# Kernel optimization log

Hardware: AMD Instinct MI355X
Metric: run time of the kernel (lower is better)

The kernel has to match this reference:

```python
import jax, jax.numpy as jnp
from jax import lax
import numpy as np

B, L, D = 2, 2048, 768
DI, DS, DTR, K = 1536, 16, 48, 4  # d_inner, d_state, dt_rank, d_conv
EPS = 1e-5


def layernorm(x, g, b):
    mu = jnp.mean(x, axis=-1, keepdims=True)
    var = jnp.mean(jnp.square(x - mu), axis=-1, keepdims=True)
    return (x - mu) * lax.rsqrt(var + EPS) * g + b


def mamba(x, in_w, conv_w, conv_b, xproj_w, dt_w, dt_b, A_log, Dp, out_w):
    # x: [B, L, D]
    xz = x @ in_w.T                       # [B, L, 2*DI]
    xc, z = jnp.split(xz, 2, axis=-1)     # [B, L, DI] each
    # causal depthwise conv1d, kernel K, left pad K-1, truncate to L
    xp = jnp.pad(xc, ((0, 0), (K - 1, 0), (0, 0)))
    conv = conv_b + sum(xp[:, k:k + L, :] * conv_w[:, k] for k in range(K))
    xc = jax.nn.silu(conv)
    dbc = xc @ xproj_w.T                  # [B, L, DTR+2*DS]
    dt = dbc[..., :DTR]
    Bm = dbc[..., DTR:DTR + DS]           # [B, L, DS]
    Cm = dbc[..., DTR + DS:]              # [B, L, DS]
    dt = jax.nn.softplus(dt @ dt_w.T + dt_b)  # [B, L, DI]
    A = -jnp.exp(A_log)                   # [DI, DS]

    def step(h, inp):
        dt_t, B_t, C_t, x_t = inp         # [B,DI], [B,DS], [B,DS], [B,DI]
        dA = jnp.exp(dt_t[..., None] * A)               # [B, DI, DS]
        h = dA * h + (dt_t * x_t)[..., None] * B_t[:, None, :]
        y = jnp.einsum('bds,bs->bd', h, C_t)
        return h, y

    h0 = jnp.zeros((x.shape[0], DI, DS), x.dtype)
    _, ys = lax.scan(step, h0, (dt.transpose(1, 0, 2), Bm.transpose(1, 0, 2),
                                Cm.transpose(1, 0, 2), xc.transpose(1, 0, 2)))
    y = ys.transpose(1, 0, 2) + xc * Dp   # [B, L, DI]
    y = y * jax.nn.silu(z)
    return y @ out_w.T                    # [B, L, D]


def setup_inputs() -> dict:
    key = jax.random.key(0)
    ks = iter(jax.random.split(key, 40))
    r = lambda s, sc=0.02: jax.random.normal(next(ks), s, jnp.float32) * sc
    A0 = jnp.log(jnp.broadcast_to(jnp.arange(1, DS + 1, dtype=jnp.float32), (DI, DS)))
    def mamba_params(p):
        return {
            f'{p}_in_w': r((2 * DI, D)), f'{p}_conv_w': r((DI, K), 0.2),
            f'{p}_conv_b': jnp.zeros((DI,)), f'{p}_xproj_w': r((DTR + 2 * DS, DI)),
            f'{p}_dt_w': r((DI, DTR), 0.1), f'{p}_dt_b': jnp.zeros((DI,)),
            f'{p}_A_log': A0, f'{p}_D': jnp.ones((DI,)), f'{p}_out_w': r((D, DI)),
        }
    inp = {'x': jax.random.normal(next(ks), (B, L, D), jnp.float32),
           'norm_g': jnp.ones((D,)), 'norm_b': jnp.zeros((D,))}
    inp.update(mamba_params('f'))
    inp.update(mamba_params('b'))
    inp.update({'mix_w': r((D, 2 * D)), 'mix_b': jnp.zeros((D,)),
                'ffn_w1': r((4 * D, D)), 'ffn_b1': jnp.zeros((4 * D,)),
                'ffn_w2': r((D, 4 * D)), 'ffn_b2': jnp.zeros((D,)),
                'ffn_norm_g': jnp.ones((D,)), 'ffn_norm_b': jnp.zeros((D,))})
    return inp


def reference(x, norm_g, norm_b,
              f_in_w, f_conv_w, f_conv_b, f_xproj_w, f_dt_w, f_dt_b, f_A_log, f_D, f_out_w,
              b_in_w, b_conv_w, b_conv_b, b_xproj_w, b_dt_w, b_dt_b, b_A_log, b_D, b_out_w,
              mix_w, mix_b, ffn_w1, ffn_b1, ffn_w2, ffn_b2, ffn_norm_g, ffn_norm_b):
    residual = x
    xn = layernorm(x, norm_g, norm_b)
    xf = mamba(xn, f_in_w, f_conv_w, f_conv_b, f_xproj_w, f_dt_w, f_dt_b, f_A_log, f_D, f_out_w)
    xb = mamba(jnp.flip(xn, axis=1), b_in_w, b_conv_w, b_conv_b, b_xproj_w,
               b_dt_w, b_dt_b, b_A_log, b_D, b_out_w)
    xb = jnp.flip(xb, axis=1)
    xm = jnp.concatenate([xf, xb], axis=-1) @ mix_w.T + mix_b
    h = xm + residual
    hn = layernorm(h, ffn_norm_g, ffn_norm_b)
    ff = jax.nn.gelu(hn @ ffn_w1.T + ffn_b1) @ ffn_w2.T + ffn_b2  # dropout = eval identity
    return ff + h
```

## Files before the change

kernel.cpp:

```cpp
#include <hip/hip_runtime.h>
#include <hip/hip_bf16.h>
#include <math.h>

#define NB 2
#define LL 2048
#define DD 768
#define DI 1536
#define DS 16
#define MM (NB*LL)
#define TCH 64
#define NCH 32
#define CONV_R 8

typedef __hip_bfloat16 bf16;
typedef __attribute__((ext_vector_type(8))) __bf16 bf16x8;
typedef __attribute__((ext_vector_type(4))) float f32x4;

__device__ __forceinline__ float b2f(bf16 v){ return __bfloat162float(v); }
__device__ __forceinline__ bf16 f2b(float v){ return __float2bfloat16(v); }
__device__ __forceinline__ float bu2f(unsigned short u){
  union {unsigned i; float f;} a; a.i = ((unsigned)u) << 16; return a.f;
}

__device__ __forceinline__ void un2(unsigned u, float& lo, float& hi){
  union {unsigned i; float f;} a, b;
  a.i = u << 16; b.i = u & 0xffff0000u;
  lo = a.f; hi = b.f;
}

__device__ __forceinline__ void async_cp16(const bf16* g, __bf16* l) {
  __builtin_amdgcn_global_load_lds((const __attribute__((address_space(1))) void*)g,
                                   (__attribute__((address_space(3))) void*)l, 16, 0, 0);
}

#define ACT_NONE 0
#define ACT_SOFTPLUS 1
#define ACT_GELU 2

__device__ __forceinline__ float apply_act(float v, int act) {
  if (act == ACT_SOFTPLUS) {
    v = (v > 15.f) ? v : log1pf(__expf(v));
  } else if (act == ACT_GELU) {
    float u = 0.7978845608028654f * (v + 0.044715f*v*v*v);
    v = 0.5f * v * (1.f + tanhf(u));
  }
  return v;
}

__global__ __launch_bounds__(512)
void gemm_kernel(const bf16* __restrict__ A, int lda,
                 const bf16* __restrict__ B, int ldb,
                 void* __restrict__ C, int ldc,
                 int N, int K,
                 const float* __restrict__ bias,
                 const float* __restrict__ addp, int ldadd,
                 int act, int f32out)
{
  __shared__ __bf16 As[128*64];
  __shared__ __bf16 Bs[128*64];
  const int tid  = threadIdx.x;
  const int lane = tid & 63, wave = tid >> 6;
  const int m0 = blockIdx.x * 128, n0 = blockIdx.y * 128;
  const int wm = wave >> 2, wn = wave & 3;

  const int srow = tid >> 3;
  const int gsw  = (tid & 7) ^ (srow & 7);
  const int scol = gsw * 8;
  const bf16* Ag[2]; const bf16* Bg[2]; int dstv[2];
  #pragma unroll
  for (int i = 0; i < 2; i++) {
    int r = srow + i*64;
    Ag[i] = A + (size_t)(m0 + r) * lda + scol;
    int br = n0 + r; if (br > N-1) br = N-1;
    Bg[i] = B + (size_t)br * ldb + scol;
    dstv[i] = r*64 + (tid & 7)*8;
  }

  f32x4 acc[4][2] = {};
  const int f = lane & 15, gq = lane >> 4, rx = lane & 7;
  const int abase = wm*64;
  const int bbase = wn*32;

  for (int kb = 0; kb < K; kb += 64) {
    __syncthreads();
    #pragma unroll
    for (int i = 0; i < 2; i++) {
      async_cp16(Ag[i] + kb, &As[dstv[i]]);
      async_cp16(Bg[i] + kb, &Bs[dstv[i]]);
    }
    __syncthreads();
    #pragma unroll
    for (int h = 0; h < 2; h++) {
      const int kk = ((h*4 + gq) ^ rx) * 8;
      bf16x8 af[4], bfr[2];
      #pragma unroll
      for (int i = 0; i < 4; i++) af[i]  = *(const bf16x8*)&As[(abase + i*16 + f)*64 + kk];
      #pragma unroll
      for (int j = 0; j < 2; j++) bfr[j] = *(const bf16x8*)&Bs[(bbase + j*16 + f)*64 + kk];
      #pragma unroll
      for (int i = 0; i < 4; i++)
        #pragma unroll
        for (int j = 0; j < 2; j++)
          acc[i][j] = __builtin_amdgcn_mfma_f32_16x16x32_bf16(af[i], bfr[j], acc[i][j], 0, 0, 0);
    }
  }

  bf16*  Cb = (bf16*)C;
  float* Cf = (float*)C;
  #pragma unroll
  for (int i = 0; i < 4; i++) {
    int rbase = m0 + wm*64 + i*16 + gq*4;
    #pragma unroll
    for (int j = 0; j < 2; j++) {
      int col = n0 + wn*32 + j*16 + f;
      if (col >= N) continue;
      float bv = bias ? bias[col] : 0.f;
      #pragma unroll
      for (int r = 0; r < 4; r++) {
        int row = rbase + r;
        float v = apply_act(acc[i][j][r] + bv, act);
        if (addp) v += addp[(size_t)row * ldadd + col];
        if (f32out) Cf[(size_t)row * ldc + col] = v;
        else        Cb[(size_t)row * ldc + col] = f2b(v);
      }
    }
  }
}

__global__ void gemm64_kernel(const bf16* __restrict__ A, int lda, size_t sA,
                              const bf16* __restrict__ B, int ldb, size_t sB,
                              void* __restrict__ C, int ldc, size_t sC,
                              int N, int K,
                              const float* __restrict__ bias0,
                              const float* __restrict__ bias1, int biasBase,
                              const float* __restrict__ addp, int ldadd,
                              int act, int f32out)
{
  __shared__ __bf16 As[64*64];
  __shared__ __bf16 Bs[64*64];
  const int tid  = threadIdx.x;
  const int lane = tid & 63, wave = tid >> 6;
  const int z = blockIdx.z;
  A += (size_t)z * sA;
  B += (size_t)z * sB;
  const float* bias = ((biasBase + z) ? bias1 : bias0);
  const int m0 = blockIdx.x * 64, n0 = blockIdx.y * 64;
  const int wm = wave & 1, wn = wave >> 1;

  const int srow = wave*16 + (lane >> 3);
  const int gsw  = (lane & 7) ^ ((lane >> 3) & 7);
  const int scol = gsw * 8;
  const bf16* Ag[2]; const bf16* Bg[2];
  __bf16 *AsW[2], *BsW[2];
  #pragma unroll
  for (int i = 0; i < 2; i++) {
    int ar = m0 + srow + i*8;
    Ag[i] = A + (size_t)ar * lda + scol;
    int br = n0 + srow + i*8; if (br > N-1) br = N-1;
    Bg[i] = B + (size_t)br * ldb + scol;
    AsW[i] = &As[(wave*16 + i*8)*64];
    BsW[i] = &Bs[(wave*16 + i*8)*64];
  }

  f32x4 acc[2][2] = {};
  const int arow = wm*32 + (lane & 15);
  const int brow = wn*32 + (lane & 15);
  const int rx = lane & 7;
  const int gq = lane >> 4;

  for (int kb = 0; kb < K; kb += 64) {
    __syncthreads();
    #pragma unroll
    for (int i = 0; i < 2; i++) {
      async_cp16(Ag[i] + kb, AsW[i]);
      async_cp16(Bg[i] + kb, BsW[i]);
    }
    __syncthreads();
    #pragma unroll
    for (int h = 0; h < 2; h++) {
      const int kk = ((h*4 + gq) ^ rx) * 8;
      bf16x8 af[2], bfr[2];
      #pragma unroll
      for (int i = 0; i < 2; i++) af[i]  = *(const bf16x8*)&As[(arow + i*16)*64 + kk];
      #pragma unroll
      for (int j = 0; j < 2; j++) bfr[j] = *(const bf16x8*)&Bs[(brow + j*16)*64 + kk];
      #pragma unroll
      for (int i = 0; i < 2; i++)
        #pragma unroll
        for (int j = 0; j < 2; j++)
          acc[i][j] = __builtin_amdgcn_mfma_f32_16x16x32_bf16(af[i], bfr[j], acc[i][j], 0, 0, 0);
    }
  }

  bf16*  Cb = (bf16*)C + z*sC;
  float* Cf = (float*)C + z*sC;
  #pragma unroll
  for (int i = 0; i < 2; i++) {
    int rbase = m0 + wm*32 + i*16 + (lane >> 4)*4;
    #pragma unroll
    for (int j = 0; j < 2; j++) {
      int col = n0 + wn*32 + j*16 + (lane & 15);
      if (col >= N) continue;
      float bv = bias ? bias[col] : 0.f;
      #pragma unroll
      for (int r = 0; r < 4; r++) {
        int row = rbase + r;
        float v = apply_act(acc[i][j][r] + bv, act);
        if (addp) v += addp[(size_t)row * ldadd + col];
        if (f32out) Cf[(size_t)row * ldc + col] = v;
        else        Cb[(size_t)row * ldc + col] = f2b(v);
      }
    }
  }
}

__global__ void ln_kernel(const float* __restrict__ x, const float* __restrict__ g,
                          const float* __restrict__ b, bf16* __restrict__ out)
{
  const int row = blockIdx.x;
  const int tid = threadIdx.x;
  const float* xr = x + (size_t)row * DD;
  float v[3], s = 0.f, s2 = 0.f;
  #pragma unroll
  for (int i = 0; i < 3; i++) {
    float f = xr[tid + i*256];
    v[i] = f; s += f; s2 += f*f;
  }
  #pragma unroll
  for (int o = 32; o > 0; o >>= 1) { s += __shfl_down(s, o, 64); s2 += __shfl_down(s2, o, 64); }
  __shared__ float ps[4], ps2[4];
  int wave = tid >> 6;
  if ((tid & 63) == 0) { ps[wave] = s; ps2[wave] = s2; }
  __syncthreads();
  s = ps[0]+ps[1]+ps[2]+ps[3]; s2 = ps2[0]+ps2[1]+ps2[2]+ps2[3];
  float mu = s * (1.f/DD);
  float var = s2 * (1.f/DD) - mu*mu;
  float rs = rsqrtf(var + 1e-5f);
  #pragma unroll
  for (int i = 0; i < 3; i++) {
    int c = tid + i*256;
    float o = (v[i] - mu) * rs * g[c] + b[c];
    out[(size_t)row * DD + c] = f2b(o);
  }
}

__global__ void conv_silu_kernel(const bf16* __restrict__ xz, int ldxz, int xzDirOff,
                                 const float* __restrict__ cw0, const float* __restrict__ cb0,
                                 const float* __restrict__ cw1, const float* __restrict__ cb1,
                                 bf16* __restrict__ xc, size_t sXc, int dirBase)
{
  const int tid = threadIdx.x;
  const int sIdx = tid / 192;
  const int lane8 = tid - sIdx*192;
  const int d8 = lane8 * 8;
  const int dir = dirBase + sIdx;
  const float* cw = dir ? cw1 : cw0;
  const float* cb = dir ? cb1 : cb0;
  float w[4][8], bb[8];
  #pragma unroll
  for (int j = 0; j < 8; j++) {
    float4 wj = *(const float4*)&cw[(d8+j)*4];
    w[0][j] = wj.x; w[1][j] = wj.y; w[2][j] = wj.z; w[3][j] = wj.w;
    bb[j] = cb[d8+j];
  }
  const int r0 = blockIdx.x * CONV_R;
  const int b = r0 >> 11, t0 = r0 & 2047;
  const bf16* base = xz + (size_t)(b*2048)*ldxz + (size_t)sIdx*xzDirOff + d8;
  bf16* out = xc + sIdx*sXc + (size_t)r0*DI + d8;
  for (int rr = 0; rr < CONV_R; rr++) {
    const int t = t0 + rr;
    float acc[8];
    #pragma unroll
    for (int j = 0; j < 8; j++) acc[j] = bb[j];
    #pragma unroll
    for (int k = 0; k < 4; k++) {
      int tt = dir ? (t + 3 - k) : (t - 3 + k);
      if (tt >= 0 && tt <= 2047) {
        union { bf16x8 v; unsigned short u[8]; } iv;
        iv.v = *(const bf16x8*)(base + (size_t)tt*ldxz);
        #pragma unroll
        for (int j = 0; j < 8; j++) acc[j] += bu2f(iv.u[j]) * w[k][j];
      }
    }
    union { bf16x8 v; bf16 e[8]; } o;
    #pragma unroll
    for (int j = 0; j < 8; j++) {
      float y = acc[j] / (1.f + __expf(-acc[j]));
      o.e[j] = f2b(y);
    }
    *(bf16x8*)(out + (size_t)rr*DI) = o.v;
  }
}

#define SZ_INW (2*DI*DD)
#define SZ_XP  (80*DI)
#define SZ_OUT (DD*DI)
#define SZ_DTW (DI*64)
#define SZ_AN  (DI*16)
#define SZ_MIX (2*DD*DD)
#define SZ_F1  (4*DD*DD)
__global__ void prep_all_kernel(const float* fi, const float* bi,
                                const float* fxp, const float* bxp,
                                const float* fo, const float* bo,
                                const float* fdt, const float* bdt,
                                const float* fa, const float* ba,
                                const float* mw, const float* f1, const float* f2,
                                bf16* w_in, bf16* w_xp2, bf16* w_out2, bf16* w_outT,
                                bf16* dtwp2, float* An2, bf16* w_mix, bf16* w_f1, bf16* w_f2)
{
  int i = blockIdx.x * 256 + threadIdx.x;
  if (i < SZ_INW) { w_in[i] = f2b(fi[i]); return; }               i -= SZ_INW;
  if (i < SZ_INW) { w_in[SZ_INW + i] = f2b(bi[i]); return; }      i -= SZ_INW;
  if (i < SZ_XP)  { w_xp2[i] = f2b(fxp[i]); return; }             i -= SZ_XP;
  if (i < SZ_XP)  { w_xp2[SZ_XP + i] = f2b(bxp[i]); return; }     i -= SZ_XP;
  if (i < SZ_OUT) { w_out2[i] = f2b(fo[i]); return; }             i -= SZ_OUT;
  if (i < SZ_OUT) { w_out2[SZ_OUT + i] = f2b(bo[i]); return; }    i -= SZ_OUT;
  if (i < SZ_OUT) { int k=i/768, p=i-k*768; w_outT[i] = f2b(fo[p*DI + k]); return; } i -= SZ_OUT;
  if (i < SZ_OUT) { int k=i/768, p=i-k*768; w_outT[SZ_OUT + i] = f2b(bo[p*DI + k]); return; } i -= SZ_OUT;
  if (i < SZ_DTW) { int r=i>>6,c=i&63; dtwp2[i] = (c<48)?f2b(fdt[r*48+c]):f2b(0.f); return; } i -= SZ_DTW;
  if (i < SZ_DTW) { int r=i>>6,c=i&63; dtwp2[SZ_DTW+i] = (c<48)?f2b(bdt[r*48+c]):f2b(0.f); return; } i -= SZ_DTW;
  if (i < SZ_AN)  { int d=i>>4,s=i&15; An2[s*DI+d] = -__expf(fa[i]); return; } i -= SZ_AN;
  if (i < SZ_AN)  { int d=i>>4,s=i&15; An2[SZ_AN + s*DI+d] = -__expf(ba[i]); return; } i -= SZ_AN;
  if (i < SZ_MIX) { w_mix[i] = f2b(mw[i]); return; }              i -= SZ_MIX;
  if (i < SZ_F1)  { w_f1[i] = f2b(f1[i]); return; }               i -= SZ_F1;
  w_f2[i] = f2b(f2[i]);
}

__global__ void scan_partial(const bf16* __restrict__ dt, size_t sDt,
                             const bf16* __restrict__ xc, size_t sXc,
                             const bf16* __restrict__ dbc, size_t sDbc,
                             const float* __restrict__ An, size_t sAn,
                             float* __restrict__ Pp, float* __restrict__ Sp,
                             int dirBase)
{
  const int tid = threadIdx.x;
  const int sIdx = blockIdx.z >> 1, b = blockIdx.z & 1;
  const int dir = dirBase + sIdx;
  const int c = blockIdx.y;
  const int d = blockIdx.x * 256 + tid;
  dt  += sIdx*sDt; xc += sIdx*sXc; dbc += sIdx*sDbc;
  const int rowbase = b*2048 + c*TCH;
  __shared__ unsigned bcs[TCH*16];
  for (int i = tid; i < TCH*16; i += 256) {
    int r = i >> 4, dw = i & 15;
    bcs[i] = ((const unsigned*)(dbc + (size_t)(rowbase + r)*96 + 48))[dw];
  }
  __syncthreads();
  float A[16], P[16], g[16];
  #pragma unroll
  for (int s = 0; s < 16; s++) { A[s] = An[sIdx*sAn + s*DI + d]; P[s] = 1.f; g[s] = 0.f; }
  int ph0 = dir ? (TCH-1) : 0;
  float dtv = b2f(dt[(size_t)(rowbase+ph0)*DI + d]);
  float xv  = b2f(xc[(size_t)(rowbase+ph0)*DI + d]);
  for (int t = 0; t < TCH; t++) {
    const int ph = dir ? (TCH-1-t) : t;
    const int tn = (t+1 < TCH) ? t+1 : t;
    const int phn = dir ? (TCH-1-tn) : tn;
    float dtn = b2f(dt[(size_t)(rowbase+phn)*DI + d]);
    float xvn = b2f(xc[(size_t)(rowbase+phn)*DI + d]);
    unsigned ub[8];
    *(uint4*)&ub[0] = *(const uint4*)&bcs[ph*16];
    *(uint4*)&ub[4] = *(const uint4*)&bcs[ph*16 + 4];
    float Bv[16];
    #pragma unroll
    for (int k = 0; k < 8; k++) un2(ub[k], Bv[2*k], Bv[2*k+1]);
    float u = dtv * xv;
    #pragma unroll
    for (int s = 0; s < 16; s++) {
      float dA = __expf(dtv * A[s]);
      P[s] *= dA;
      g[s] = dA * g[s] + u * Bv[s];
    }
    dtv = dtn; xv = xvn;
  }
  size_t base = ((((size_t)sIdx*NB + b)*NCH + c)*DI + d) * 16;
  #pragma unroll
  for (int s = 0; s < 16; s++) { Pp[base+s] = P[s]; Sp[base+s] = g[s]; }
}

__global__ void scan_combine(const float* __restrict__ Pp, const float* __restrict__ Sp,
                             float* __restrict__ h0, int dirBase)
{
  const int j = blockIdx.x * 256 + threadIdx.x;
  const int b = blockIdx.y;
  const int sIdx = blockIdx.z;
  const int dir = dirBase + sIdx;
  float h = 0.f;
  for (int k = 0; k < NCH; k++) {
    int c = dir ? (NCH-1-k) : k;
    size_t idx = (((size_t)sIdx*NB + b)*NCH + c)*DI*16 + j;
    h0[idx] = h;
    h = Pp[idx]*h + Sp[idx];
  }
}

__global__ void scan_final(const bf16* __restrict__ dt, size_t sDt,
                           const bf16* __restrict__ xc, size_t sXc,
                           const bf16* __restrict__ dbc, size_t sDbc,
                           const bf16* __restrict__ xz, int ldxz, int xzDirOff,
                           const float* __restrict__ An, size_t sAn,
                           const float* __restrict__ Dp0, const float* __restrict__ Dp1,
                           const float* __restrict__ h0,
                           bf16* __restrict__ yout, int ldY, size_t sY, int dirBase)
{
  const int tid = threadIdx.x;
  const int sIdx = blockIdx.z >> 1, b = blockIdx.z & 1;
  const int dir = dirBase + sIdx;
  const int c = blockIdx.y;
  const int d = blockIdx.x * 256 + tid;
  dt += sIdx*sDt; xc += sIdx*sXc; dbc += sIdx*sDbc; yout += sIdx*sY;
  const float* Dp = dir ? Dp1 : Dp0;
  const int rowbase = b*2048 + c*TCH;
  __shared__ unsigned bcs[TCH*16];
  for (int i = tid; i < TCH*16; i += 256) {
    int r = i >> 4, dw = i & 15;
    bcs[i] = ((const unsigned*)(dbc + (size_t)(rowbase + r)*96 + 48))[dw];
  }
  __syncthreads();
  float A[16], h[16];
  size_t hbase = ((((size_t)sIdx*NB + b)*NCH + c)*DI + d) * 16;
  #pragma unroll
  for (int s = 0; s < 16; s++) { A[s] = An[sIdx*sAn + s*DI + d]; h[s] = h0[hbase+s]; }
  const float Dd = Dp[d];
  const bf16* zp = xz + sIdx*xzDirOff + DI + d;
  int ph0 = dir ? (TCH-1) : 0;
  float dtv = b2f(dt[(size_t)(rowbase+ph0)*DI + d]);
  float xv  = b2f(xc[(size_t)(rowbase+ph0)*DI + d]);
  float zv  = b2f(zp[(size_t)(rowbase+ph0)*ldxz]);
  for (int t = 0; t < TCH; t++) {
    const int ph = dir ? (TCH-1-t) : t;
    const int row = rowbase + ph;
    const int tn = (t+1 < TCH) ? t+1 : t;
    const int phn = dir ? (TCH-1-tn) : tn;
    float dtn = b2f(dt[(size_t)(rowbase+phn)*DI + d]);
    float xvn = b2f(xc[(size_t)(rowbase+phn)*DI + d]);
    float zvn = b2f(zp[(size_t)(rowbase+phn)*ldxz]);
    unsigned ub[8], uc[8];
    *(uint4*)&ub[0] = *(const uint4*)&bcs[ph*16];
    *(uint4*)&ub[4] = *(const uint4*)&bcs[ph*16 + 4];
    *(uint4*)&uc[0] = *(const uint4*)&bcs[ph*16 + 8];
    *(uint4*)&uc[4] = *(const uint4*)&bcs[ph*16 + 12];
    float Bv[16], Cv[16];
    #pragma unroll
    for (int k = 0; k < 8; k++) { un2(ub[k], Bv[2*k], Bv[2*k+1]); un2(uc[k], Cv[2*k], Cv[2*k+1]); }
    float u = dtv * xv;
    float y = 0.f;
    #pragma unroll
    for (int s = 0; s < 16; s++) {
      float dA = __expf(dtv * A[s]);
      h[s] = dA * h[s] + u * Bv[s];
      y += h[s] * Cv[s];
    }
    float yg = (y + xv * Dd) * (zv / (1.f + __expf(-zv)));
    yout[(size_t)row*ldY + d] = f2b(yg);
    dtv = dtn; xv = xvn; zv = zvn;
  }
}

extern "C" void kernel_launch(void* const* d_in, const int* in_sizes, int n_in,
                              void* d_out, int out_size, void* d_ws, size_t ws_size,
                              hipStream_t stream)
{
  const float* x      = (const float*)d_in[0];
  const float* norm_g = (const float*)d_in[1];
  const float* norm_b = (const float*)d_in[2];
  const float* fi  = (const float*)d_in[3];
  const float* fcw = (const float*)d_in[4];
  const float* fcb = (const float*)d_in[5];
  const float* fxp = (const float*)d_in[6];
  const float* fdt = (const float*)d_in[7];
  const float* fdb = (const float*)d_in[8];
  const float* fa  = (const float*)d_in[9];
  const float* fD  = (const float*)d_in[10];
  const float* fo  = (const float*)d_in[11];
  const float* bi  = (const float*)d_in[12];
  const float* bcw = (const float*)d_in[13];
  const float* bcb = (const float*)d_in[14];
  const float* bxp = (const float*)d_in[15];
  const float* bdt = (const float*)d_in[16];
  const float* bdb = (const float*)d_in[17];
  const float* ba  = (const float*)d_in[18];
  const float* bD  = (const float*)d_in[19];
  const float* bo  = (const float*)d_in[20];
  const float* mix_w  = (const float*)d_in[21];
  const float* mix_b  = (const float*)d_in[22];
  const float* ffn_w1 = (const float*)d_in[23];
  const float* ffn_b1 = (const float*)d_in[24];
  const float* ffn_w2 = (const float*)d_in[25];
  const float* ffn_b2 = (const float*)d_in[26];
  const float* ffn_ng = (const float*)d_in[27];
  const float* ffn_nb = (const float*)d_in[28];

  auto al = [](size_t x){ return (x + 255) & ~(size_t)255; };
  const size_t fixedB =
      al((size_t)2*SZ_AN*4) + al((size_t)2*SZ_DTW*2) + al((size_t)2*SZ_INW*2) +
      al((size_t)2*SZ_XP*2) + al((size_t)2*SZ_OUT*2) + al((size_t)2*SZ_OUT*2) +
      al((size_t)SZ_MIX*2) + al((size_t)SZ_F1*2) + al((size_t)SZ_F1*2) +
      al((size_t)MM*DD*2) + al((size_t)MM*DI*2);
  const size_t concB = fixedB + al((size_t)MM*2*DI*2*2) + 2*al((size_t)2*MM*DI*2) +
      al((size_t)2*MM*96*2) + 3*al((size_t)2*NB*NCH*DI*16*4) +
      al((size_t)MM*2*DI*2) + al((size_t)DD*2*DI*2);
  const bool conc = (ws_size >= concB);

  size_t o = 0;
  char* wsb = (char*)d_ws;
  auto nxt = [&](size_t bytes) -> char* {
    char* p = wsb + o; o += (bytes + 255) & ~(size_t)255; return p;
  };
  float* An2   = (float*)nxt((size_t)2*SZ_AN*4);
  bf16*  dtwp2 = (bf16*) nxt((size_t)2*SZ_DTW*2);
  bf16*  w_in  = (bf16*) nxt((size_t)2*SZ_INW*2);
  bf16*  w_xp2 = (bf16*) nxt((size_t)2*SZ_XP*2);
  bf16*  w_out2= (bf16*) nxt((size_t)2*SZ_OUT*2);
  bf16*  w_outT= (bf16*) nxt((size_t)2*SZ_OUT*2);
  bf16*  w_mix = (bf16*) nxt((size_t)SZ_MIX*2);
  bf16*  w_f1  = (bf16*) nxt((size_t)SZ_F1*2);
  bf16*  w_f2  = (bf16*) nxt((size_t)SZ_F1*2);
  bf16*  xn    = (bf16*) nxt((size_t)MM*DD*2);
  bf16*  xfb   = (bf16*) nxt((size_t)MM*DI*2);

  bf16 *xz, *xc, *dtb, *dbc, *ybuf = nullptr, *Gp = nullptr;
  float *Pp, *Sp, *h0, *hbuf;
  int ldxz, xzDirOff;
  size_t sXc, sDbc, sDt;
  if (conc) {
    xz  = (bf16*) nxt((size_t)MM*2*DI*2*2);
    xc  = (bf16*) nxt((size_t)2*MM*DI*2);
    dtb = (bf16*) nxt((size_t)2*MM*DI*2);
    dbc = (bf16*) nxt((size_t)2*MM*96*2);
    Pp  = (float*)nxt((size_t)2*NB*NCH*DI*16*4);
    Sp  = (float*)nxt((size_t)2*NB*NCH*DI*16*4);
    h0  = (float*)nxt((size_t)2*NB*NCH*DI*16*4);
    ybuf= (bf16*) nxt((size_t)MM*2*DI*2);
    Gp  = (bf16*) nxt((size_t)DD*2*DI*2);
    hbuf = Pp;
    ldxz = 2*2*DI; xzDirOff = 2*DI;
    sXc = (size_t)MM*DI; sDbc = (size_t)MM*96; sDt = (size_t)MM*DI;
  } else {
    xz  = (bf16*) nxt((size_t)MM*2*DI*2);
    xc  = (bf16*) nxt((size_t)MM*DI*2);
    dtb = (bf16*) nxt((size_t)MM*DI*2);
    dbc = (bf16*) nxt((size_t)MM*96*2);
    Pp  = (float*)nxt((size_t)NB*NCH*DI*16*4);
    Sp  = (float*)nxt((size_t)NB*NCH*DI*16*4);
    h0  = (float*)nxt((size_t)NB*NCH*DI*16*4);
    hbuf = (float*)dtb;
    ldxz = 2*DI; xzDirOff = 0;
    sXc = 0; sDbc = 0; sDt = 0;
  }
  bf16* hn = xn;
  bf16* a1 = xz;

  const int prepN = 2*SZ_INW + 2*SZ_XP + 4*SZ_OUT + 2*SZ_DTW + 2*SZ_AN + SZ_MIX + 2*SZ_F1;
  prep_all_kernel<<<(prepN + 255)/256, 256, 0, stream>>>(
      fi, bi, fxp, bxp, fo, bo, fdt, bdt, fa, ba, mix_w, ffn_w1, ffn_w2,
      w_in, w_xp2, w_out2, w_outT, dtwp2, An2, w_mix, w_f1, w_f2);

  if (conc) {
    gemm64_kernel<<<dim3(12, 24, 2), 256, 0, stream>>>(w_mix, 2*DD, (size_t)DD,
                                                       w_outT, DD, (size_t)SZ_OUT,
                                                       Gp, 2*DI, (size_t)DI, DI, DD,
                                                       nullptr, nullptr, 0, nullptr, 0, ACT_NONE, 0);
  }

  ln_kernel<<<MM, 256, 0, stream>>>(x, norm_g, norm_b, xn);

  if (conc) {
    gemm_kernel<<<dim3(32, 48), 512, 0, stream>>>(xn, DD, w_in, DD, xz, ldxz,
                                                  2*2*DI, DD, nullptr, nullptr, 0,
                                                  ACT_NONE, 0);
    conv_silu_kernel<<<MM/CONV_R, 384, 0, stream>>>(xz, ldxz, xzDirOff,
                                                    fcw, fcb, bcw, bcb, xc, sXc, 0);
    gemm64_kernel<<<dim3(64, 2, 2), 256, 0, stream>>>(xc, DI, sXc, w_xp2, DI, (size_t)SZ_XP,
                                                      dbc, 96, sDbc, 80, DI,
                                                      nullptr, nullptr, 0, nullptr, 0, ACT_NONE, 0);
    gemm64_kernel<<<dim3(64, 24, 2), 256, 0, stream>>>(dbc, 96, sDbc, dtwp2, 64, (size_t)SZ_DTW,
                                                       dtb, DI, sDt, DI, 64,
                                                       fdb, bdb, 0, nullptr, 0, ACT_SOFTPLUS, 0);
    scan_partial<<<dim3(DI/256, NCH, 4), 256, 0, stream>>>(dtb, sDt, xc, sXc, dbc, sDbc,
                                                           An2, (size_t)SZ_AN, Pp, Sp, 0);
    scan_combine<<<dim3(DI*16/256, NB, 2), 256, 0, stream>>>(Pp, Sp, h0, 0);
    scan_final<<<dim3(DI/256, NCH, 4), 256, 0, stream>>>(dtb, sDt, xc, sXc, dbc, sDbc,
                                                         xz, ldxz, xzDirOff, An2, (size_t)SZ_AN,
                                                         fD, bD, h0, ybuf, 2*DI, (size_t)DI, 0);
    gemm64_kernel<<<dim3(64, 12, 1), 256, 0, stream>>>(ybuf, 2*DI, 0, Gp, 2*DI, 0,
                                                       hbuf, DD, 0, DD, 2*DI,
                                                       mix_b, mix_b, 0, x, DD, ACT_NONE, 1);
  } else {
    for (int dir = 0; dir < 2; ++dir) {
      gemm_kernel<<<dim3(32, 24), 512, 0, stream>>>(xn, DD, w_in + (size_t)dir*SZ_INW, DD,
                                                    xz, ldxz, 2*DI, DD, nullptr, nullptr, 0,
                                                    ACT_NONE, 0);
      conv_silu_kernel<<<MM/CONV_R, 192, 0, stream>>>(xz, ldxz, 0,
                                                      fcw, fcb, bcw, bcb, xc, 0, dir);
      gemm64_kernel<<<dim3(64, 2, 1), 256, 0, stream>>>(xc, DI, 0, w_xp2 + (size_t)dir*SZ_XP, DI, 0,
                                                        dbc, 96, 0, 80, DI,
                                                        nullptr, nullptr, 0, nullptr, 0, ACT_NONE, 0);
      gemm64_kernel<<<dim3(64, 24, 1), 256, 0, stream>>>(dbc, 96, 0, dtwp2 + (size_t)dir*SZ_DTW, 64, 0,
                                                         dtb, DI, 0, DI, 64,
                                                         fdb, bdb, dir, nullptr, 0, ACT_SOFTPLUS, 0);
      scan_partial<<<dim3(DI/256, NCH, 2), 256, 0, stream>>>(dtb, 0, xc, 0, dbc, 0,
                                                             An2 + (size_t)dir*SZ_AN, 0, Pp, Sp, dir);
      scan_combine<<<dim3(DI*16/256, NB, 1), 256, 0, stream>>>(Pp, Sp, h0, dir);
      scan_final<<<dim3(DI/256, NCH, 2), 256, 0, stream>>>(dtb, 0, xc, 0, dbc, 0,
                                                           xz, ldxz, 0, An2 + (size_t)dir*SZ_AN, 0,
                                                           fD, bD, h0, xc, DI, 0, dir);
      gemm64_kernel<<<dim3(64, 12, 1), 256, 0, stream>>>(xc, DI, 0, w_out2 + (size_t)dir*SZ_OUT, DI, 0,
                                                         (void*)((bf16*)xfb + dir*DD), 2*DD, 0, DD, DI,
                                                         nullptr, nullptr, 0, nullptr, 0, ACT_NONE, 0);
    }
    gemm64_kernel<<<dim3(64, 12, 1), 256, 0, stream>>>(xfb, 2*DD, 0, w_mix, 2*DD, 0,
                                                       hbuf, DD, 0, DD, 2*DD,
                                                       mix_b, mix_b, 0, x, DD, ACT_NONE, 1);
  }

  ln_kernel<<<MM, 256, 0, stream>>>(hbuf, ffn_ng, ffn_nb, hn);
  gemm_kernel<<<dim3(32, 24), 512, 0, stream>>>(hn, DD, w_f1, DD, a1, 4*DD,
                                                4*DD, DD, ffn_b1, nullptr, 0, ACT_GELU, 0);
  gemm64_kernel<<<dim3(64, 12, 1), 256, 0, stream>>>(a1, 4*DD, 0, w_f2, 4*DD, 0,
                                                     d_out, DD, 0, DD, 4*DD,
                                                     ffn_b2, ffn_b2, 0, hbuf, DD, ACT_NONE, 1);
}
```

Baseline: 565.6 us.

## Split scan state across four lanes per channel and fold log2e into A

The chunked selective scan kernels now assign four threads to each inner channel, each owning four of the sixteen state entries. This raises the block count by four and cuts per-thread registers, at the cost of redundant dt/x/z loads and a two-step shuffle reduction for y in the final pass. A is prescaled by log2(e) at weight prep so exp2f replaces __expf, and partial/state buffers are read and written as float4 vectors.

```diff
diff --git a/kernel.cpp b/kernel.cpp
--- a/kernel.cpp
+++ b/kernel.cpp
@@ -11,6 +11,7 @@
 #define TCH 64
 #define NCH 32
 #define CONV_R 8
+#define LOG2E 1.4426950408889634f
 
 typedef __hip_bfloat16 bf16;
 typedef __attribute__((ext_vector_type(8))) __bf16 bf16x8;
@@ -319,8 +320,8 @@
   if (i < SZ_OUT) { int k=i/768, p=i-k*768; w_outT[SZ_OUT + i] = f2b(bo[p*DI + k]); return; } i -= SZ_OUT;
   if (i < SZ_DTW) { int r=i>>6,c=i&63; dtwp2[i] = (c<48)?f2b(fdt[r*48+c]):f2b(0.f); return; } i -= SZ_DTW;
   if (i < SZ_DTW) { int r=i>>6,c=i&63; dtwp2[SZ_DTW+i] = (c<48)?f2b(bdt[r*48+c]):f2b(0.f); return; } i -= SZ_DTW;
-  if (i < SZ_AN)  { int d=i>>4,s=i&15; An2[s*DI+d] = -__expf(fa[i]); return; } i -= SZ_AN;
-  if (i < SZ_AN)  { int d=i>>4,s=i&15; An2[SZ_AN + s*DI+d] = -__expf(ba[i]); return; } i -= SZ_AN;
+  if (i < SZ_AN)  { int d=i>>4,s=i&15; An2[s*DI+d] = -__expf(fa[i]) * LOG2E; return; } i -= SZ_AN;
+  if (i < SZ_AN)  { int d=i>>4,s=i&15; An2[SZ_AN + s*DI+d] = -__expf(ba[i]) * LOG2E; return; } i -= SZ_AN;
   if (i < SZ_MIX) { w_mix[i] = f2b(mw[i]); return; }              i -= SZ_MIX;
   if (i < SZ_F1)  { w_f1[i] = f2b(f1[i]); return; }               i -= SZ_F1;
   w_f2[i] = f2b(f2[i]);
@@ -337,45 +338,46 @@
   const int sIdx = blockIdx.z >> 1, b = blockIdx.z & 1;
   const int dir = dirBase + sIdx;
   const int c = blockIdx.y;
-  const int d = blockIdx.x * 256 + tid;
+  const int dLoc = tid >> 2, sq = tid & 3;
+  const int d = blockIdx.x * 64 + dLoc;
   dt  += sIdx*sDt; xc += sIdx*sXc; dbc += sIdx*sDbc;
   const int rowbase = b*2048 + c*TCH;
-  __shared__ unsigned bcs[TCH*16];
-  for (int i = tid; i < TCH*16; i += 256) {
-    int r = i >> 4, dw = i & 15;
+  __shared__ unsigned bcs[TCH*8];
+  for (int i = tid; i < TCH*8; i += 256) {
+    int r = i >> 3, dw = i & 7;
     bcs[i] = ((const unsigned*)(dbc + (size_t)(rowbase + r)*96 + 48))[dw];
   }
   __syncthreads();
-  float A[16], P[16], g[16];
-  #pragma unroll
-  for (int s = 0; s < 16; s++) { A[s] = An[sIdx*sAn + s*DI + d]; P[s] = 1.f; g[s] = 0.f; }
-  int ph0 = dir ? (TCH-1) : 0;
-  float dtv = b2f(dt[(size_t)(rowbase+ph0)*DI + d]);
-  float xv  = b2f(xc[(size_t)(rowbase+ph0)*DI + d]);
+  float A[4]; f32x4 P, g;
+  #pragma unroll
+  for (int j = 0; j < 4; j++) { A[j] = An[sIdx*sAn + (sq*4+j)*DI + d]; P[j] = 1.f; g[j] = 0.f; }
+  const bf16* dtp = dt + (size_t)rowbase*DI + d;
+  const bf16* xcp = xc + (size_t)rowbase*DI + d;
+  const int step = dir ? -DI : DI;
+  int off = dir ? (TCH-1)*DI : 0;
+  float dtv = b2f(dtp[off]);
+  float xv  = b2f(xcp[off]);
   for (int t = 0; t < TCH; t++) {
     const int ph = dir ? (TCH-1-t) : t;
-    const int tn = (t+1 < TCH) ? t+1 : t;
-    const int phn = dir ? (TCH-1-tn) : tn;
-    float dtn = b2f(dt[(size_t)(rowbase+phn)*DI + d]);
-    float xvn = b2f(xc[(size_t)(rowbase+phn)*DI + d]);
-    unsigned ub[8];
-    *(uint4*)&ub[0] = *(const uint4*)&bcs[ph*16];
-    *(uint4*)&ub[4] = *(const uint4*)&bcs[ph*16 + 4];
-    float Bv[16];
-    #pragma unroll
-    for (int k = 0; k < 8; k++) un2(ub[k], Bv[2*k], Bv[2*k+1]);
+    const int offn = (t+1 < TCH) ? off + step : off;
+    float dtn = b2f(dtp[offn]);
+    float xvn = b2f(xcp[offn]);
+    uint2 ub = *(const uint2*)&bcs[ph*8 + sq*2];
+    float Bv[4];
+    un2(ub.x, Bv[0], Bv[1]);
+    un2(ub.y, Bv[2], Bv[3]);
     float u = dtv * xv;
     #pragma unroll
-    for (int s = 0; s < 16; s++) {
-      float dA = __expf(dtv * A[s]);
-      P[s] *= dA;
-      g[s] = dA * g[s] + u * Bv[s];
-    }
-    dtv = dtn; xv = xvn;
-  }
-  size_t base = ((((size_t)sIdx*NB + b)*NCH + c)*DI + d) * 16;
-  #pragma unroll
-  for (int s = 0; s < 16; s++) { Pp[base+s] = P[s]; Sp[base+s] = g[s]; }
+    for (int j = 0; j < 4; j++) {
+      float dA = exp2f(dtv * A[j]);
+      P[j] *= dA;
+      g[j] = dA * g[j] + u * Bv[j];
+    }
+    off = offn; dtv = dtn; xv = xvn;
+  }
+  size_t base = ((((size_t)sIdx*NB + b)*NCH + c)*DI + d) * 16 + sq*4;
+  *(f32x4*)&Pp[base] = P;
+  *(f32x4*)&Sp[base] = g;
 }
 
 __global__ void scan_combine(const float* __restrict__ Pp, const float* __restrict__ Sp,
@@ -407,7 +409,8 @@
   const int sIdx = blockIdx.z >> 1, b = blockIdx.z & 1;
   const int dir = dirBase + sIdx;
   const int c = blockIdx.y;
-  const int d = blockIdx.x * 256 + tid;
+  const int dLoc = tid >> 2, sq = tid & 3;
+  const int d = blockIdx.x * 64 + dLoc;
   dt += sIdx*sDt; xc += sIdx*sXc; dbc += sIdx*sDbc; yout += sIdx*sY;
   const float* Dp = dir ? Dp1 : Dp0;
   const int rowbase = b*2048 + c*TCH;
@@ -417,43 +420,51 @@
     bcs[i] = ((const unsigned*)(dbc + (size_t)(rowbase + r)*96 + 48))[dw];
   }
   __syncthreads();
-  float A[16], h[16];
-  size_t hbase = ((((size_t)sIdx*NB + b)*NCH + c)*DI + d) * 16;
-  #pragma unroll
-  for (int s = 0; s < 16; s++) { A[s] = An[sIdx*sAn + s*DI + d]; h[s] = h0[hbase+s]; }
+  float A[4]; f32x4 h;
+  size_t hbase = ((((size_t)sIdx*NB + b)*NCH + c)*DI + d) * 16 + sq*4;
+  h = *(const f32x4*)&h0[hbase];
+  #pragma unroll
+  for (int j = 0; j < 4; j++) A[j] = An[sIdx*sAn + (sq*4+j)*DI + d];
   const float Dd = Dp[d];
-  const bf16* zp = xz + sIdx*xzDirOff + DI + d;
-  int ph0 = dir ? (TCH-1) : 0;
-  float dtv = b2f(dt[(size_t)(rowbase+ph0)*DI + d]);
-  float xv  = b2f(xc[(size_t)(rowbase+ph0)*DI + d]);
-  float zv  = b2f(zp[(size_t)(rowbase+ph0)*ldxz]);
+  const bf16* dtp = dt + (size_t)rowbase*DI + d;
+  const bf16* xcp = xc + (size_t)rowbase*DI + d;
+  const bf16* zp  = xz + (size_t)rowbase*ldxz + sIdx*xzDirOff + DI + d;
+  const int step = dir ? -DI : DI;
+  const int zstep = dir ? -ldxz : ldxz;
+  int off  = dir ? (TCH-1)*DI : 0;
+  int zoff = dir ? (TCH-1)*ldxz : 0;
+  float dtv = b2f(dtp[off]);
+  float xv  = b2f(xcp[off]);
+  float zv  = b2f(zp[zoff]);
   for (int t = 0; t < TCH; t++) {
     const int ph = dir ? (TCH-1-t) : t;
     const int row = rowbase + ph;
-    const int tn = (t+1 < TCH) ? t+1 : t;
-    const int phn = dir ? (TCH-1-tn) : tn;
-    float dtn = b2f(dt[(size_t)(rowbase+phn)*DI + d]);
-    float xvn = b2f(xc[(size_t)(rowbase+phn)*DI + d]);
-    float zvn = b2f(zp[(size_t)(rowbase+phn)*ldxz]);
-    unsigned ub[8], uc[8];
-    *(uint4*)&ub[0] = *(const uint4*)&bcs[ph*16];
-    *(uint4*)&ub[4] = *(const uint4*)&bcs[ph*16 + 4];
-    *(uint4*)&uc[0] = *(const uint4*)&bcs[ph*16 + 8];
-    *(uint4*)&uc[4] = *(const uint4*)&bcs[ph*16 + 12];
-    float Bv[16], Cv[16];
-    #pragma unroll
-    for (int k = 0; k < 8; k++) { un2(ub[k], Bv[2*k], Bv[2*k+1]); un2(uc[k], Cv[2*k], Cv[2*k+1]); }
+    const bool last = (t+1 >= TCH);
+    const int offn  = last ? off  : off + step;
+    const int zoffn = last ? zoff : zoff + zstep;
+    float dtn = b2f(dtp[offn]);
+    float xvn = b2f(xcp[offn]);
+    float zvn = b2f(zp[zoffn]);
+    uint2 ub = *(const uint2*)&bcs[ph*16 + sq*2];
+    uint2 uc = *(const uint2*)&bcs[ph*16 + 8 + sq*2];
+    float Bv[4], Cv[4];
+    un2(ub.x, Bv[0], Bv[1]); un2(ub.y, Bv[2], Bv[3]);
+    un2(uc.x, Cv[0], Cv[1]); un2(uc.y, Cv[2], Cv[3]);
     float u = dtv * xv;
     float y = 0.f;
     #pragma unroll
-    for (int s = 0; s < 16; s++) {
-      float dA = __expf(dtv * A[s]);
-      h[s] = dA * h[s] + u * Bv[s];
-      y += h[s] * Cv[s];
-    }
-    float yg = (y + xv * Dd) * (zv / (1.f + __expf(-zv)));
-    yout[(size_t)row*ldY + d] = f2b(yg);
-    dtv = dtn; xv = xvn; zv = zvn;
+    for (int j = 0; j < 4; j++) {
+      float dA = exp2f(dtv * A[j]);
+      h[j] = dA * h[j] + u * Bv[j];
+      y += h[j] * Cv[j];
+    }
+    y += __shfl_xor(y, 1, 64);
+    y += __shfl_xor(y, 2, 64);
+    if (sq == 0) {
+      float yg = (y + xv * Dd) * (zv / (1.f + __expf(-zv)));
+      yout[(size_t)row*ldY + d] = f2b(yg);
+    }
+    off = offn; zoff = zoffn; dtv = dtn; xv = xvn; zv = zvn;
   }
 }
 
@@ -577,12 +588,12 @@
     gemm64_kernel<<<dim3(64, 24, 2), 256, 0, stream>>>(dbc, 96, sDbc, dtwp2, 64, (size_t)SZ_DTW,
                                                        dtb, DI, sDt, DI, 64,
                                                        fdb, bdb, 0, nullptr, 0, ACT_SOFTPLUS, 0);
-    scan_partial<<<dim3(DI/256, NCH, 4), 256, 0, stream>>>(dtb, sDt, xc, sXc, dbc, sDbc,
-                                                           An2, (size_t)SZ_AN, Pp, Sp, 0);
+    scan_partial<<<dim3(DI/64, NCH, 4), 256, 0, stream>>>(dtb, sDt, xc, sXc, dbc, sDbc,
+                                                          An2, (size_t)SZ_AN, Pp, Sp, 0);
     scan_combine<<<dim3(DI*16/256, NB, 2), 256, 0, stream>>>(Pp, Sp, h0, 0);
-    scan_final<<<dim3(DI/256, NCH, 4), 256, 0, stream>>>(dtb, sDt, xc, sXc, dbc, sDbc,
-                                                         xz, ldxz, xzDirOff, An2, (size_t)SZ_AN,
-                                                         fD, bD, h0, ybuf, 2*DI, (size_t)DI, 0);
+    scan_final<<<dim3(DI/64, NCH, 4), 256, 0, stream>>>(dtb, sDt, xc, sXc, dbc, sDbc,
+                                                        xz, ldxz, xzDirOff, An2, (size_t)SZ_AN,
+                                                        fD, bD, h0, ybuf, 2*DI, (size_t)DI, 0);
     gemm64_kernel<<<dim3(64, 12, 1), 256, 0, stream>>>(ybuf, 2*DI, 0, Gp, 2*DI, 0,
                                                        hbuf, DD, 0, DD, 2*DI,
                                                        mix_b, mix_b, 0, x, DD, ACT_NONE, 1);
@@ -599,12 +610,12 @@
       gemm64_kernel<<<dim3(64, 24, 1), 256, 0, stream>>>(dbc, 96, 0, dtwp2 + (size_t)dir*SZ_DTW, 64, 0,
                                                          dtb, DI, 0, DI, 64,
                                                          fdb, bdb, dir, nullptr, 0, ACT_SOFTPLUS, 0);
-      scan_partial<<<dim3(DI/256, NCH, 2), 256, 0, stream>>>(dtb, 0, xc, 0, dbc, 0,
-                                                             An2 + (size_t)dir*SZ_AN, 0, Pp, Sp, dir);
+      scan_partial<<<dim3(DI/64, NCH, 2), 256, 0, stream>>>(dtb, 0, xc, 0, dbc, 0,
+                                                            An2 + (size_t)dir*SZ_AN, 0, Pp, Sp, dir);
       scan_combine<<<dim3(DI*16/256, NB, 1), 256, 0, stream>>>(Pp, Sp, h0, dir);
-      scan_final<<<dim3(DI/256, NCH, 2), 256, 0, stream>>>(dtb, 0, xc, 0, dbc, 0,
-                                                           xz, ldxz, 0, An2 + (size_t)dir*SZ_AN, 0,
-                                                           fD, bD, h0, xc, DI, 0, dir);
+      scan_final<<<dim3(DI/64, NCH, 2), 256, 0, stream>>>(dtb, 0, xc, 0, dbc, 0,
+                                                          xz, ldxz, 0, An2 + (size_t)dir*SZ_AN, 0,
+                                                          fD, bD, h0, xc, DI, 0, dir);
       gemm64_kernel<<<dim3(64, 12, 1), 256, 0, stream>>>(xc, DI, 0, w_out2 + (size_t)dir*SZ_OUT, DI, 0,
                                                          (void*)((bf16*)xfb + dir*DD), 2*DD, 0, DD, DI,
                                                          nullptr, nullptr, 0, nullptr, 0, ACT_NONE, 0);
```

Measured after the change: 664.7 us. +17.5%, slower.
